# Kernel optimization log

Hardware: AMD Instinct MI355X
Metric: run time of the kernel (lower is better)

Reference implementation:

```python
import jax, jax.numpy as jnp
import numpy as np

S = 7          # grid size
C = 10         # num classes (SVHN digits)
L_COORD = 5.0
L_NOOBJ = 0.5
EPS = 1e-6     # safe-sqrt epsilon (original sqrt(clamp(x,0,1)) has inf grad at 0)


def _iou(b1, b2):
    """Vectorized translation of computeIOU. b1, b2: [..., 4] as (left, top, w, h)."""
    l1l, l1t, w1, h1 = b1[..., 0], b1[..., 1], b1[..., 2], b1[..., 3]
    l2l, l2t, w2, h2 = b2[..., 0], b2[..., 1], b2[..., 2], b2[..., 3]
    l1r, l1b = l1l + w1, l1t + h1
    l2r, l2b = l2l + w2, l2t + h2
    a1 = w1 * h1
    a2 = w2 * h2
    cont_by2 = (l2l <= l1l) & (l2t <= l1t) & (l2r >= l1r) & (l2b >= l1b)  # box2 contains box1
    cont_by1 = (l1l <= l2l) & (l1t <= l2t) & (l1r >= l2r) & (l1b >= l2b)  # box1 contains box2
    sep = (l1r <= l2l) | (l2r <= l1l) | (l1b <= l2t) | (l2b <= l1t)       # disjoint
    iw = jnp.minimum(l1r, l2r) - jnp.maximum(l1l, l2l)
    ih = jnp.minimum(l1b, l2b) - jnp.maximum(l1t, l2t)
    inter = iw * ih
    gen = inter / (a1 + a2 - inter)
    return jnp.where(cont_by2, a1 / a2,
           jnp.where(cont_by1, a2 / a1,
           jnp.where(sep, jnp.zeros_like(gen), gen)))


def setup_inputs() -> dict:
    key = jax.random.key(0)
    k1, k2, k3, k4 = jax.random.split(key, 4)
    N = 16384
    pred_tensor = jax.random.normal(k1, (N, S, S, 20), dtype=jnp.float32)
    xywh = jax.random.uniform(k2, (N, S, S, 4), dtype=jnp.float32)
    conf = (jax.random.uniform(k3, (N, S, S, 1)) < 0.15).astype(jnp.float32)  # ~7 objects/img
    cls = jax.random.randint(k4, (N, S, S, 1), 0, C).astype(jnp.float32)
    target_tensor = jnp.concatenate([xywh, conf, cls], axis=-1)
    return {"pred_tensor": pred_tensor, "target_tensor": target_tensor}


def reference(pred_tensor, target_tensor):
    N = pred_tensor.shape[0]
    conf_t = target_tensor[..., 4]                       # [N,S,S]
    coo = (conf_t > 0).astype(pred_tensor.dtype)
    noo = (conf_t == 0).astype(pred_tensor.dtype)

    # no-object confidence loss: both predicted confidences vs target conf (=0 on noo cells)
    noobj_loss = jnp.sum(noo * ((pred_tensor[..., 4] - conf_t) ** 2 +
                                (pred_tensor[..., 9] - conf_t) ** 2))

    # responsible-box selection via IoU (vectorized replacement of the python loop)
    bt = target_tensor[..., :4]                          # target box [N,S,S,4]
    bp0 = pred_tensor[..., 0:5]
    bp1 = pred_tensor[..., 5:10]
    iou0 = _iou(bp0[..., :4], bt)
    iou1 = _iou(bp1[..., :4], bt)
    pick0 = iou0 >= iou1                                 # box0 responsible when tie or higher
    max_iou = jax.lax.stop_gradient(jnp.where(pick0, iou0, iou1))  # Variable() detach in orig
    resp = jnp.where(pick0[..., None], bp0, bp1)         # responsible pred box [N,S,S,5]
    nonresp = jnp.where(pick0[..., None], bp1, bp0)

    contain_loss = jnp.sum(coo * (resp[..., 4] - max_iou) ** 2)

    xy_p = jnp.clip(resp[..., :2], 0.0, 1.0)
    xy_t = jnp.clip(bt[..., :2], 0.0, 1.0)
    wh_p = jnp.sqrt(jnp.clip(resp[..., 2:4], EPS, 1.0))
    wh_t = jnp.sqrt(jnp.clip(bt[..., 2:4], EPS, 1.0))
    loc_loss = jnp.sum(coo[..., None] * ((xy_p - xy_t) ** 2 + (wh_p - wh_t) ** 2))

    not_contain_loss = jnp.sum(coo * nonresp[..., 4] ** 2)  # target conf forced to 0

    # class cross-entropy (sum reduction) over object cells
    logits = pred_tensor[..., 10:]                       # [N,S,S,10]
    logz = jax.nn.logsumexp(logits, axis=-1)
    cls_idx = target_tensor[..., 5].astype(jnp.int32)
    picked = jnp.take_along_axis(logits, cls_idx[..., None], axis=-1)[..., 0]
    class_loss = jnp.sum(coo * (logz - picked))

    total = (L_COORD * loc_loss + 2.0 * contain_loss + not_contain_loss +
             L_NOOBJ * noobj_loss + class_loss)
    return total / N
```

## Files before the change

kernel.cpp:

```cpp
#include <hip/hip_runtime.h>


#define SBLK 1024

constexpr float L_COORD = 5.0f;
constexpr float L_NOOBJ = 0.5f;
constexpr float EPS_    = 1e-6f;

__device__ __forceinline__ float clamp01(float x) { return fminf(fmaxf(x, 0.0f), 1.0f); }

__device__ __forceinline__ float iou_f(float l1l, float l1t, float w1, float h1,
                                       float l2l, float l2t, float w2, float h2) {
    float l1r = l1l + w1, l1b = l1t + h1;
    float l2r = l2l + w2, l2b = l2t + h2;
    float a1 = w1 * h1, a2 = w2 * h2;
    bool cont_by2 = (l2l <= l1l) && (l2t <= l1t) && (l2r >= l1r) && (l2b >= l1b);
    bool cont_by1 = (l1l <= l2l) && (l1t <= l2t) && (l1r >= l2r) && (l1b >= l2b);
    bool sep = (l1r <= l2l) || (l2r <= l1l) || (l1b <= l2t) || (l2b <= l1t);
    float iw = fminf(l1r, l2r) - fmaxf(l1l, l2l);
    float ih = fminf(l1b, l2b) - fmaxf(l1t, l2t);
    float inter = iw * ih;
    float gen = inter * __builtin_amdgcn_rcpf(a1 + a2 - inter);
    float r = sep ? 0.0f : gen;
    r = cont_by1 ? a2 * __builtin_amdgcn_rcpf(a1) : r;
    r = cont_by2 ? a1 * __builtin_amdgcn_rcpf(a2) : r;
    return r;
}

__global__ __launch_bounds__(SBLK) void yolo_loss_kernel(
        const float* __restrict__ pred, const float* __restrict__ tgt,
        double* __restrict__ partials, int ncells) {
    int i = blockIdx.x * SBLK + threadIdx.x;
    float total = 0.0f;
    if (i < ncells) {
        const float4* p4 = reinterpret_cast<const float4*>(pred + (size_t)i * 20);
        float4 pa = p4[0];
        float4 pb = p4[1];
        float4 pc = p4[2];
        float4 pd = p4[3];
        float4 pe = p4[4];
        const float2* t2 = reinterpret_cast<const float2*>(tgt + (size_t)i * 6);
        float2 t0 = t2[0];
        float2 t1 = t2[1];
        float2 tc = t2[2];

        float conf = tc.x;
        float coo = (conf > 0.0f) ? 1.0f : 0.0f;
        float noo = (conf == 0.0f) ? 1.0f : 0.0f;

        float d0 = pb.x - conf, d1 = pc.y - conf;
        float noobj = noo * (d0 * d0 + d1 * d1);

        float b0l = pa.x, b0t = pa.y, b0w = pa.z, b0h = pa.w, b0c = pb.x;
        float b1l = pb.y, b1t = pb.z, b1w = pb.w, b1h = pc.x, b1c = pc.y;
        float btl = t0.x, btt = t0.y, btw = t1.x, bth = t1.y;

        float iou0 = iou_f(b0l, b0t, b0w, b0h, btl, btt, btw, bth);
        float iou1 = iou_f(b1l, b1t, b1w, b1h, btl, btt, btw, bth);
        bool pick0 = (iou0 >= iou1);
        float max_iou = pick0 ? iou0 : iou1;

        float rl = pick0 ? b0l : b1l;
        float rt = pick0 ? b0t : b1t;
        float rw = pick0 ? b0w : b1w;
        float rh = pick0 ? b0h : b1h;
        float rc = pick0 ? b0c : b1c;
        float nc = pick0 ? b1c : b0c;

        float cd = rc - max_iou;
        float contain = cd * cd;
        float not_contain = nc * nc;

        float ex = clamp01(rl) - clamp01(btl);
        float ey = clamp01(rt) - clamp01(btt);
        float sw = __builtin_amdgcn_sqrtf(fminf(fmaxf(rw, EPS_), 1.0f))
                 - __builtin_amdgcn_sqrtf(fminf(fmaxf(btw, EPS_), 1.0f));
        float sh = __builtin_amdgcn_sqrtf(fminf(fmaxf(rh, EPS_), 1.0f))
                 - __builtin_amdgcn_sqrtf(fminf(fmaxf(bth, EPS_), 1.0f));
        float loc = ex * ex + ey * ey + sw * sw + sh * sh;

        float lg0 = pc.z, lg1 = pc.w;
        float lg2 = pd.x, lg3 = pd.y, lg4 = pd.z, lg5 = pd.w;
        float lg6 = pe.x, lg7 = pe.y, lg8 = pe.z, lg9 = pe.w;
        float m = fmaxf(lg0, lg1);
        m = fmaxf(m, fmaxf(lg2, lg3));
        m = fmaxf(m, fmaxf(lg4, lg5));
        m = fmaxf(m, fmaxf(lg6, lg7));
        m = fmaxf(m, fmaxf(lg8, lg9));
        float ssum = __expf(lg0 - m) + __expf(lg1 - m) + __expf(lg2 - m) +
                     __expf(lg3 - m) + __expf(lg4 - m) + __expf(lg5 - m) +
                     __expf(lg6 - m) + __expf(lg7 - m) + __expf(lg8 - m) +
                     __expf(lg9 - m);
        float logz = m + __logf(ssum);
        int ci = (int)tc.y;
        float picked = lg0;
        picked = (ci == 1) ? lg1 : picked;
        picked = (ci == 2) ? lg2 : picked;
        picked = (ci == 3) ? lg3 : picked;
        picked = (ci == 4) ? lg4 : picked;
        picked = (ci == 5) ? lg5 : picked;
        picked = (ci == 6) ? lg6 : picked;
        picked = (ci == 7) ? lg7 : picked;
        picked = (ci == 8) ? lg8 : picked;
        picked = (ci == 9) ? lg9 : picked;
        float cls_loss = logz - picked;

        total = L_COORD * (coo * loc)
              + 2.0f * (coo * contain)
              + (coo * not_contain)
              + L_NOOBJ * noobj
              + coo * cls_loss;
    }

    float v = total;
    #pragma unroll
    for (int off = 32; off > 0; off >>= 1)
        v += __shfl_down(v, off, 64);
    __shared__ float smw[SBLK / 64];
    int lane = threadIdx.x & 63;
    int wid  = threadIdx.x >> 6;
    if (lane == 0) smw[wid] = v;
    __syncthreads();
    if (threadIdx.x == 0) {
        double s = 0.0;
        #pragma unroll
        for (int w = 0; w < SBLK / 64; ++w) s += (double)smw[w];
        partials[blockIdx.x] = s;
    }
}

#define RBLK 1024

__global__ __launch_bounds__(RBLK) void yolo_reduce_kernel(
        const double* __restrict__ partials, int nparts,
        float* __restrict__ out, double invN) {
    double v = 0.0;
    for (int idx = threadIdx.x; idx < nparts; idx += RBLK)
        v += partials[idx];
    #pragma unroll
    for (int off = 32; off > 0; off >>= 1)
        v += __shfl_down(v, off, 64);
    __shared__ double sm[RBLK / 64];
    int lane = threadIdx.x & 63;
    int wid  = threadIdx.x >> 6;
    if (lane == 0) sm[wid] = v;
    __syncthreads();
    if (threadIdx.x == 0) {
        double s = 0.0;
        #pragma unroll
        for (int w = 0; w < RBLK / 64; ++w) s += sm[w];
        out[0] = (float)(s * invN);
    }
}

extern "C" void kernel_launch(void* const* d_in, const int* in_sizes, int n_in,
                              void* d_out, int out_size, void* d_ws, size_t ws_size,
                              hipStream_t stream) {
    const float* pred = (const float*)d_in[0];
    const float* tgt  = (const float*)d_in[1];
    int ncells = in_sizes[0] / 20;
    int N = ncells / 49;

    int nblocks = (ncells + SBLK - 1) / SBLK;
    yolo_loss_kernel<<<nblocks, SBLK, 0, stream>>>(pred, tgt, (double*)d_ws, ncells);
    yolo_reduce_kernel<<<1, RBLK, 0, stream>>>((const double*)d_ws, nblocks,
                                               (float*)d_out, 1.0 / (double)N);
}
```

Baseline: 21.88 us.

## Stage per-wave cell data through LDS for coalesced global loads

Each wave loads its 64 cells' prediction and target data as consecutive float4/float2 chunks, so lanes read contiguous addresses. It then transposes the data through shared memory so each lane gets its own cell's fields. This targets the strided 80-byte-per-lane access pattern of the original loads. The block size also drops to 256, and the change adds LDS traffic plus a barrier.

```diff
diff --git a/kernel.cpp b/kernel.cpp
--- a/kernel.cpp
+++ b/kernel.cpp
@@ -1,7 +1,9 @@
 #include <hip/hip_runtime.h>
 
 
-#define SBLK 1024
+#define SBLK 256
+#define WPB  (SBLK / 64)
+#define CPW  64
 
 constexpr float L_COORD = 5.0f;
 constexpr float L_NOOBJ = 0.5f;
@@ -30,20 +32,49 @@
 __global__ __launch_bounds__(SBLK) void yolo_loss_kernel(
         const float* __restrict__ pred, const float* __restrict__ tgt,
         double* __restrict__ partials, int ncells) {
-    int i = blockIdx.x * SBLK + threadIdx.x;
+    __shared__ float4 sp[WPB][CPW * 5];
+    __shared__ float2 st[WPB][CPW * 3];
+
+    const int lane = threadIdx.x & 63;
+    const int wid  = threadIdx.x >> 6;
+    const int wave_cell0 = (blockIdx.x * WPB + wid) * CPW;
+    const int cell = wave_cell0 + lane;
+
+    const float4* p4g = reinterpret_cast<const float4*>(pred);
+    const float2* t2g = reinterpret_cast<const float2*>(tgt);
+    const int maxp4 = ncells * 5 - 1;
+    const int maxt2 = ncells * 3 - 1;
+    const int pbase = wave_cell0 * 5;
+    const int tbase = wave_cell0 * 3;
+
+    float4 pr[5];
+    #pragma unroll
+    for (int k = 0; k < 5; ++k)
+        pr[k] = p4g[min(pbase + k * CPW + lane, maxp4)];
+    float2 tr[3];
+    #pragma unroll
+    for (int k = 0; k < 3; ++k)
+        tr[k] = t2g[min(tbase + k * CPW + lane, maxt2)];
+
+    #pragma unroll
+    for (int k = 0; k < 5; ++k)
+        sp[wid][k * CPW + lane] = pr[k];
+    #pragma unroll
+    for (int k = 0; k < 3; ++k)
+        st[wid][k * CPW + lane] = tr[k];
+    __syncthreads();
+
+    float4 pa = sp[wid][lane * 5 + 0];
+    float4 pb = sp[wid][lane * 5 + 1];
+    float4 pc = sp[wid][lane * 5 + 2];
+    float4 pd = sp[wid][lane * 5 + 3];
+    float4 pe = sp[wid][lane * 5 + 4];
+    float2 t0 = st[wid][lane * 3 + 0];
+    float2 t1 = st[wid][lane * 3 + 1];
+    float2 tc = st[wid][lane * 3 + 2];
+
     float total = 0.0f;
-    if (i < ncells) {
-        const float4* p4 = reinterpret_cast<const float4*>(pred + (size_t)i * 20);
-        float4 pa = p4[0];
-        float4 pb = p4[1];
-        float4 pc = p4[2];
-        float4 pd = p4[3];
-        float4 pe = p4[4];
-        const float2* t2 = reinterpret_cast<const float2*>(tgt + (size_t)i * 6);
-        float2 t0 = t2[0];
-        float2 t1 = t2[1];
-        float2 tc = t2[2];
-
+    {
         float conf = tc.x;
         float coo = (conf > 0.0f) ? 1.0f : 0.0f;
         float noo = (conf == 0.0f) ? 1.0f : 0.0f;
@@ -110,21 +141,20 @@
               + (coo * not_contain)
               + L_NOOBJ * noobj
               + coo * cls_loss;
+        total = (cell < ncells) ? total : 0.0f;
     }
 
     float v = total;
     #pragma unroll
     for (int off = 32; off > 0; off >>= 1)
         v += __shfl_down(v, off, 64);
-    __shared__ float smw[SBLK / 64];
-    int lane = threadIdx.x & 63;
-    int wid  = threadIdx.x >> 6;
+    __shared__ float smw[WPB];
     if (lane == 0) smw[wid] = v;
     __syncthreads();
     if (threadIdx.x == 0) {
         double s = 0.0;
         #pragma unroll
-        for (int w = 0; w < SBLK / 64; ++w) s += (double)smw[w];
+        for (int w = 0; w < WPB; ++w) s += (double)smw[w];
         partials[blockIdx.x] = s;
     }
 }
```

New measurement: 22.22 us. About the same (+1.6%).
